# Kernel tuning notes

Measured on AMD Instinct MI355X. Metric: run time of the kernel, lower is better.

The kernel has to match this reference:

```python
import jax, jax.numpy as jnp
import numpy as np
from jax import lax

PAD_ID = 0
V, E = 100000, 300          # word vocab / embedding dim
VC, EC, C = 100, 50, 100    # char vocab / char emb dim / char conv channels
H, L = 256, 17              # lstm hidden / n_labels
B, S, LC = 32, 128, 50


def _conv1d(x, w, b):
    # x [B, Cin, T], w [Cout, Cin, K] -> valid conv
    y = lax.conv_general_dilated(x, w, window_strides=(1,), padding='VALID',
                                 dimension_numbers=('NCH', 'OIH', 'NCH'))
    return y + b[None, :, None]


def _lstm_dir(x_sbd, w_ih, w_hh, b, h0, c0):
    # x_sbd [S,B,D]; PyTorch gate order i,f,g,o
    def step(carry, x_t):
        h, c = carry
        g = x_t @ w_ih.T + h @ w_hh.T + b
        i, f, gg, o = jnp.split(g, 4, axis=-1)
        c = jax.nn.sigmoid(f) * c + jax.nn.sigmoid(i) * jnp.tanh(gg)
        h = jax.nn.sigmoid(o) * jnp.tanh(c)
        return (h, c), h
    _, hs = lax.scan(step, (h0, c0), x_sbd)
    return hs  # [S,B,H]


def _emissions(x, x_char, word_emb, char_emb,
               conv1_w, conv1_b, conv2_w, conv2_b, conv3_w, conv3_b,
               w_ih_f, w_hh_f, b_f, w_ih_b, w_hh_b, b_b, h0, c0, fc_w, fc_b):
    emb = word_emb[x]                                   # [B,S,E]
    ce = char_emb[x_char].transpose(0, 2, 1)            # [B,EC,LC]
    ce = jax.nn.relu(_conv1d(ce, conv1_w, conv1_b))
    ce = jax.nn.relu(_conv1d(ce, conv2_w, conv2_b))
    ce = jax.nn.relu(_conv1d(ce, conv3_w, conv3_b))
    pooled = ce.max(axis=2)                             # [B,C] (max over time)
    char_rep = jnp.broadcast_to(pooled[:, None, :], (emb.shape[0], emb.shape[1], pooled.shape[1]))
    xin = jnp.concatenate([emb, char_rep], axis=2)      # [B,S,E+C]
    xs = xin.transpose(1, 0, 2)                         # [S,B,D]
    hf = _lstm_dir(xs, w_ih_f, w_hh_f, b_f, h0[0], c0[0])
    hb = _lstm_dir(xs[::-1], w_ih_b, w_hh_b, b_b, h0[1], c0[1])[::-1]
    hcat = jnp.concatenate([hf, hb], axis=-1).transpose(1, 0, 2)  # [B,S,2H]
    em = hcat @ fc_w.T + fc_b                           # [B,S,L]
    return jax.nn.softmax(em, axis=1)                   # faithful: softmax over seq dim


def _viterbi(emissions, mask, start_t, trans, end_t):
    # emissions [B,S,L], mask [B,S]
    em = emissions.transpose(1, 0, 2)                   # [S,B,L]
    m = mask.T                                          # [S,B]
    score0 = start_t[None, :] + em[0]                   # [B,L]

    def fwd(score, inp):
        e_t, m_t = inp
        cand = score[:, :, None] + trans[None] + e_t[:, None, :]  # [B,L,L]
        nscore = cand.max(axis=1)
        idx = cand.argmax(axis=1).astype(jnp.int32)
        score = jnp.where(m_t[:, None] > 0, nscore, score)
        return score, idx

    score, hist = lax.scan(fwd, score0, (em[1:], m[1:]))  # hist [S-1,B,L]
    score = score + end_t[None, :]
    last = jnp.argmax(score, axis=-1).astype(jnp.int32)   # [B]

    def back(cur, inp):
        h_t, m_t = inp
        prev = jnp.take_along_axis(h_t, cur[:, None], axis=1)[:, 0]
        cur = jnp.where(m_t > 0, prev, cur)
        return cur, cur

    _, tags_rev = lax.scan(back, last, (hist[::-1], m[1:][::-1]))
    tags = jnp.concatenate([tags_rev[::-1], last[None]], axis=0)  # [S,B]
    return tags.T                                                 # [B,S]


def setup_inputs() -> dict:
    key = jax.random.key(0)
    ks = jax.random.split(key, 24)
    f = lambda i, shape, s=0.1: (jax.random.normal(ks[i], shape, dtype=jnp.float32) * s)
    inp = {
        'x': jax.random.randint(ks[0], (B, S), 1, V),          # no PAD -> mask all ones
        'x_char': jax.random.randint(ks[1], (B, LC), 1, VC),
        'word_emb': f(2, (V, E), 1.0),
        'char_emb': f(3, (VC, EC), 1.0).at[PAD_ID].set(0.0),
        'conv1_w': f(4, (C, EC, 3)), 'conv1_b': f(5, (C,)),
        'conv2_w': f(6, (C, C, 4)), 'conv2_b': f(7, (C,)),
        'conv3_w': f(8, (C, C, 5)), 'conv3_b': f(9, (C,)),
        'w_ih_f': f(10, (4 * H, E + C)), 'w_hh_f': f(11, (4 * H, H)), 'b_f': f(12, (4 * H,)),
        'w_ih_b': f(13, (4 * H, E + C)), 'w_hh_b': f(14, (4 * H, H)), 'b_b': f(15, (4 * H,)),
        'h0': f(16, (2, B, H), 1.0), 'c0': f(17, (2, B, H), 1.0),
        'fc_w': f(18, (L, 2 * H)), 'fc_b': f(19, (L,)),
        'start_t': f(20, (L,)), 'trans': f(21, (L, L)), 'end_t': f(22, (L,)),
    }
    return inp


def reference(x, x_char, word_emb, char_emb, conv1_w, conv1_b, conv2_w, conv2_b,
              conv3_w, conv3_b, w_ih_f, w_hh_f, b_f, w_ih_b, w_hh_b, b_b,
              h0, c0, fc_w, fc_b, start_t, trans, end_t):
    mask = (x != PAD_ID).astype(jnp.float32)
    em = _emissions(x, x_char, word_emb, char_emb, conv1_w, conv1_b, conv2_w, conv2_b,
                    conv3_w, conv3_b, w_ih_f, w_hh_f, b_f, w_ih_b, w_hh_b, b_b,
                    h0, c0, fc_w, fc_b)
    return _viterbi(em, mask, start_t, trans, end_t)
```

## Files before the change

kernel.cpp:

```cpp
#include <hip/hip_runtime.h>
#include <cmath>

#define B_   32
#define S_   128
#define E_   300
#define C_   100
#define EC_  50
#define LC_  50
#define H_   256
#define G4_  1024
#define L_   17
#define DHID_ 400
#define NBLKD 8
#define SLAB_ 8192
#define SENT2_ 0x7E007E00u

typedef _Float16 half8 __attribute__((ext_vector_type(8)));
typedef float f32x4 __attribute__((ext_vector_type(4)));
typedef unsigned long long ull;
struct __align__(16) U2 { ull x, y; };

__device__ __forceinline__ unsigned pack_split(float v) {
  _Float16 hi = (fabsf(v) >= 6.104e-5f) ? (_Float16)v : (_Float16)0.0f;
  float hif = (float)hi;
  _Float16 lo = (_Float16)((v - hif) * 2048.0f);
  return (unsigned)__builtin_bit_cast(unsigned short, hi)
       | ((unsigned)__builtin_bit_cast(unsigned short, lo) << 16);
}

__global__ void k_hinit(const float* __restrict__ h0, unsigned* __restrict__ hfrag) {
  int idx = blockIdx.x * 256 + threadIdx.x;
  const int total = 2 * (S_ + 1) * SLAB_;
  if (idx >= total) return;
  int sd = idx / SLAB_;
  int within = idx % SLAB_;
  int t = sd % (S_ + 1), d = sd / (S_ + 1);
  if (t != 0) { hfrag[idx] = SENT2_; return; }
  int m8 = within & 7;
  int lane = (within >> 3) & 63;
  int q = within >> 9;
  int Kt = q & 7, Nt = q >> 3;
  int m = m8 & 3, isLo = m8 >> 2;
  int k0 = Kt * 32 + (lane >> 4) * 8 + 2 * m;
  int b = Nt * 16 + (lane & 15);
  unsigned p0 = pack_split(h0[((size_t)d * B_ + b) * H_ + k0]);
  unsigned p1 = pack_split(h0[((size_t)d * B_ + b) * H_ + k0 + 1]);
  unsigned hiw = (p0 & 0xFFFFu) | (p1 << 16);
  unsigned low = (p0 >> 16) | (p1 & 0xFFFF0000u);
  hfrag[idx] = isLo ? low : hiw;
}

__global__ void k_conv1(const int* __restrict__ x_char, const float* __restrict__ char_emb,
                        const float* __restrict__ w1, const float* __restrict__ b1,
                        float* __restrict__ out1) {
  int b = blockIdx.x;
  int ot = blockIdx.y;
  __shared__ float ce[EC_ * 52];
  __shared__ float wl[50 * 150];
  __shared__ int ids[LC_];
  int tid = threadIdx.x;
  if (tid < LC_) ids[tid] = x_char[b * LC_ + tid];
  __syncthreads();
  for (int idx = tid; idx < LC_ * EC_; idx += 256) {
    int t = idx / EC_, ec = idx % EC_;
    ce[ec * 52 + t] = char_emb[ids[t] * EC_ + ec];
  }
  int obase = ot * 50;
  for (int idx = tid; idx < 50 * 150; idx += 256)
    wl[idx] = w1[obase * 150 + idx];
  __syncthreads();
  for (int idx = tid; idx < 50 * 48; idx += 256) {
    int o = idx / 48, t = idx % 48;
    float acc = b1[obase + o];
    const float* wr = &wl[o * 150];
    for (int c = 0; c < EC_; ++c) {
      const float* ip = &ce[c * 52 + t];
      acc += wr[c * 3 + 0] * ip[0] + wr[c * 3 + 1] * ip[1] + wr[c * 3 + 2] * ip[2];
    }
    out1[((size_t)b * C_ + obase + o) * 48 + t] = fmaxf(acc, 0.0f);
  }
}

__global__ void k_conv2(const float* __restrict__ in, const float* __restrict__ w2,
                        const float* __restrict__ b2, float* __restrict__ out2) {
  int b = blockIdx.x, ot = blockIdx.y;
  __shared__ float il[C_ * 48];
  __shared__ float wl[25 * 400];
  int tid = threadIdx.x;
  for (int idx = tid; idx < C_ * 48; idx += 256) il[idx] = in[(size_t)b * C_ * 48 + idx];
  int obase = ot * 25;
  for (int idx = tid; idx < 25 * 400; idx += 256) wl[idx] = w2[obase * 400 + idx];
  __syncthreads();
  for (int idx = tid; idx < 25 * 45; idx += 256) {
    int o = idx / 45, t = idx % 45;
    float acc = b2[obase + o];
    const float* wr = &wl[o * 400];
    for (int c = 0; c < C_; ++c) {
      const float* ip = &il[c * 48 + t];
      acc += wr[c * 4 + 0] * ip[0] + wr[c * 4 + 1] * ip[1] +
             wr[c * 4 + 2] * ip[2] + wr[c * 4 + 3] * ip[3];
    }
    out2[((size_t)b * C_ + obase + o) * 45 + t] = fmaxf(acc, 0.0f);
  }
}

__global__ void k_conv3(const float* __restrict__ in, const float* __restrict__ w3,
                        const float* __restrict__ b3, float* __restrict__ pooled) {
  int b = blockIdx.x, ot = blockIdx.y;
  __shared__ float il[C_ * 45];
  __shared__ float wl[20 * 500];
  __shared__ float o3[20 * 44];
  int tid = threadIdx.x;
  for (int idx = tid; idx < C_ * 45; idx += 256) il[idx] = in[(size_t)b * C_ * 45 + idx];
  int obase = ot * 20;
  for (int idx = tid; idx < 20 * 500; idx += 256) wl[idx] = w3[obase * 500 + idx];
  __syncthreads();
  for (int idx = tid; idx < 20 * 41; idx += 256) {
    int o = idx / 41, t = idx % 41;
    float acc = b3[obase + o];
    const float* wr = &wl[o * 500];
    for (int c = 0; c < C_; ++c) {
      const float* ip = &il[c * 45 + t];
      acc += wr[c * 5 + 0] * ip[0] + wr[c * 5 + 1] * ip[1] + wr[c * 5 + 2] * ip[2] +
             wr[c * 5 + 3] * ip[3] + wr[c * 5 + 4] * ip[4];
    }
    o3[o * 44 + t] = fmaxf(acc, 0.0f);
  }
  __syncthreads();
  if (tid < 20) {
    float m = o3[tid * 44];
    for (int t = 1; t < 41; ++t) m = fmaxf(m, o3[tid * 44 + t]);
    pooled[b * C_ + obase + tid] = m;
  }
}

__global__ void k_biaseff(const float* __restrict__ pooled,
                          const float* __restrict__ w_ih_f, const float* __restrict__ b_f,
                          const float* __restrict__ w_ih_b, const float* __restrict__ b_b,
                          float* __restrict__ biaseff) {
  int b = blockIdx.x, d = blockIdx.y;
  const float* wih = d ? w_ih_b : w_ih_f;
  const float* bb = d ? b_b : b_f;
  __shared__ float pl[C_];
  int tid = threadIdx.x;
  if (tid < C_) pl[tid] = pooled[b * C_ + tid];
  __syncthreads();
  for (int j = tid; j < G4_; j += 256) {
    float acc = bb[j];
    const float* wr = &wih[(size_t)j * DHID_ + E_];
    for (int c = 0; c < C_; ++c) acc += pl[c] * wr[c];
    biaseff[((size_t)d * G4_ + j) * B_ + b] = acc;
  }
}

__global__ __launch_bounds__(256) void k_gemm_in(
    const int* __restrict__ x, const float* __restrict__ word_emb,
    const float* __restrict__ w_ih_f, const float* __restrict__ w_ih_b,
    const float* __restrict__ biaseff, float* __restrict__ gi) {
  int jt = blockIdx.x;
  int rt = blockIdx.y;
  int d = blockIdx.z;
  const float* wih = d ? w_ih_b : w_ih_f;
  __shared__ float Al[16][132];
  __shared__ float Bl[16][132];
  __shared__ int wid[128];
  int tid = threadIdx.x;
  int r0 = rt * 128, j0 = jt * 128;
  if (tid < 128) {
    int r = r0 + tid;
    int t = r >> 5, b = r & 31;
    wid[tid] = x[b * S_ + t];
  }
  __syncthreads();
  float acc[8][8];
#pragma unroll
  for (int i = 0; i < 8; ++i)
#pragma unroll
    for (int j = 0; j < 8; ++j) acc[i][j] = 0.f;
  int ty = tid >> 4, tx = tid & 15;

  for (int k0 = 0; k0 < 304; k0 += 16) {
#pragma unroll
    for (int i = 0; i < 2; ++i) {
      int f = tid + i * 256;
      int rl = f >> 2, kc = f & 3;
      const float* src = word_emb + (size_t)wid[rl] * E_;
#pragma unroll
      for (int e = 0; e < 4; ++e) {
        int k = k0 + kc * 4 + e;
        float v = src[k < E_ ? k : (E_ - 1)];
        Al[kc * 4 + e][rl] = (k < E_) ? v : 0.f;
      }
    }
#pragma unroll
    for (int i = 0; i < 2; ++i) {
      int f = tid + i * 256;
      int jl = f >> 2, kc = f & 3;
      const float* src = wih + (size_t)(j0 + jl) * DHID_;
#pragma unroll
      for (int e = 0; e < 4; ++e) {
        int k = k0 + kc * 4 + e;
        float v = src[k];
        Bl[kc * 4 + e][jl] = (k < E_) ? v : 0.f;
      }
    }
    __syncthreads();
#pragma unroll
    for (int kk = 0; kk < 16; ++kk) {
      float4 a0 = *(const float4*)(&Al[kk][ty * 8]);
      float4 a1 = *(const float4*)(&Al[kk][ty * 8 + 4]);
      float4 b0 = *(const float4*)(&Bl[kk][tx * 8]);
      float4 b1 = *(const float4*)(&Bl[kk][tx * 8 + 4]);
      float av[8] = {a0.x, a0.y, a0.z, a0.w, a1.x, a1.y, a1.z, a1.w};
      float bv[8] = {b0.x, b0.y, b0.z, b0.w, b1.x, b1.y, b1.z, b1.w};
#pragma unroll
      for (int i = 0; i < 8; ++i)
#pragma unroll
        for (int j = 0; j < 8; ++j) acc[i][j] = fmaf(av[i], bv[j], acc[i][j]);
    }
    __syncthreads();
  }
  int b0 = (ty & 3) * 8;
  int tt = rt * 4 + (ty >> 2);
#pragma unroll
  for (int jj = 0; jj < 8; ++jj) {
    int j = j0 + tx * 8 + jj;
    const float* be = biaseff + ((size_t)d * G4_ + j) * B_ + b0;
    float4 bl = *(const float4*)(be);
    float4 bh = *(const float4*)(be + 4);
    float4 lo, hi;
    lo.x = acc[0][jj] + bl.x; lo.y = acc[1][jj] + bl.y;
    lo.z = acc[2][jj] + bl.z; lo.w = acc[3][jj] + bl.w;
    hi.x = acc[4][jj] + bh.x; hi.y = acc[5][jj] + bh.y;
    hi.z = acc[6][jj] + bh.z; hi.w = acc[7][jj] + bh.w;
    float* dst = gi + (((size_t)(d * S_ + tt) * G4_) + j) * B_ + b0;
    *(float4*)dst = lo;
    *(float4*)(dst + 4) = hi;
  }
}

__global__ __launch_bounds__(256, 1) void k_lstm(
    const float* __restrict__ w_hh_f, const float* __restrict__ w_hh_b,
    const float* __restrict__ c0, const float* __restrict__ gi,
    float* __restrict__ hbuf, unsigned* __restrict__ hfrag) {
  const int iblk = blockIdx.x;
  const int d = blockIdx.y;
  const float* whh = d ? w_hh_b : w_hh_f;
  const int tid = threadIdx.x;
  const int w = tid >> 6;
  const int l = tid & 63;
  const int lx = l & 15, lq = l >> 4;
  const int u0 = iblk * 32;

  __shared__ ull slh[2048];
  __shared__ ull sll[2048];
  __shared__ float gl[4 * 32 * 33];
  __shared__ unsigned ps[2 * 576];

  half8 whi[2][8], wlo[2][8];
#pragma unroll
  for (int Mt = 0; Mt < 2; ++Mt) {
#pragma unroll
    for (int Kt = 0; Kt < 8; ++Kt) {
      int row = w * H_ + u0 + Mt * 16 + lx;
      int kk0 = Kt * 32 + lq * 8;
      const float* src = whh + (size_t)row * H_ + kk0;
      float4 f0 = *(const float4*)src;
      float4 f1 = *(const float4*)(src + 4);
      float wv[8] = {f0.x, f0.y, f0.z, f0.w, f1.x, f1.y, f1.z, f1.w};
      union { unsigned short s[8]; half8 h; } HI, LO;
#pragma unroll
      for (int j = 0; j < 8; ++j) {
        float v = wv[j];
        _Float16 hi = (fabsf(v) >= 6.104e-5f) ? (_Float16)v : (_Float16)0.0f;
        float hif = (float)hi;
        _Float16 lo = (_Float16)((v - hif) * 2048.0f);
        HI.s[j] = __builtin_bit_cast(unsigned short, hi);
        LO.s[j] = __builtin_bit_cast(unsigned short, lo);
      }
      whi[Mt][Kt] = HI.h;
      wlo[Mt][Kt] = LO.h;
    }
  }

  const int bc = tid & 31, cw = tid >> 5;
  float creg[4];
#pragma unroll
  for (int cu = 0; cu < 4; ++cu)
    creg[cu] = c0[((size_t)d * B_ + bc) * H_ + u0 + cu * 8 + cw];

  const int pNt = bc >> 4;
  const int pm = cw >> 1;
  const bool phi = (cw & 1) == 0;
  const int plane = bc & 15;
  const float inv2048 = 1.0f / 2048.0f;

  for (int t = 0; t < S_; ++t) {
    int torig = d ? (S_ - 1 - t) : t;

    f32x4 acch[2][2], accl[2][2];
    {
      const float* gbase = gi + ((size_t)(d * S_ + torig) * G4_) * B_;
#pragma unroll
      for (int Mt = 0; Mt < 2; ++Mt)
#pragma unroll
        for (int Nt = 0; Nt < 2; ++Nt) {
          f32x4 v;
#pragma unroll
          for (int r = 0; r < 4; ++r) {
            int j = w * H_ + u0 + Mt * 16 + lq * 4 + r;
            v[r] = gbase[(size_t)j * B_ + Nt * 16 + lx];
          }
          acch[Mt][Nt] = v;
          f32x4 z = {0.f, 0.f, 0.f, 0.f};
          accl[Mt][Nt] = z;
        }
    }

    const ull* hp = (const ull*)(hfrag + (size_t)(d * (S_ + 1) + t) * SLAB_);
    ull pv[4][4];
#pragma unroll
    for (int c = 0; c < 4; ++c) {
      size_t base = ((size_t)(w * 4 + c) * 64 + l) * 4;
#pragma unroll
      for (int j = 0; j < 4; ++j)
        pv[c][j] = __hip_atomic_load(&hp[base + j], __ATOMIC_RELAXED,
                                     __HIP_MEMORY_SCOPE_AGENT);
    }
    for (;;) {
      bool pending = false;
#pragma unroll
      for (int c = 0; c < 4; ++c)
#pragma unroll
        for (int j = 0; j < 4; ++j)
          pending |= ((unsigned)pv[c][j] == SENT2_) |
                     ((unsigned)(pv[c][j] >> 32) == SENT2_);
      if (!pending) break;
#pragma unroll
      for (int c = 0; c < 4; ++c) {
        size_t base = ((size_t)(w * 4 + c) * 64 + l) * 4;
#pragma unroll
        for (int j = 0; j < 4; ++j)
          pv[c][j] = __hip_atomic_load(&hp[base + j], __ATOMIC_RELAXED,
                                       __HIP_MEMORY_SCOPE_AGENT);
      }
    }
#pragma unroll
    for (int c = 0; c < 4; ++c) {
      int idx = ((w * 4 + c) * 64 + l) * 2;
      U2 vh; vh.x = pv[c][0]; vh.y = pv[c][1];
      U2 vl; vl.x = pv[c][2]; vl.y = pv[c][3];
      *(U2*)&slh[idx] = vh;
      *(U2*)&sll[idx] = vl;
    }
    __syncthreads();

#pragma unroll
    for (int Kt = 0; Kt < 8; ++Kt) {
      half8 Bhi[2], Blo[2];
#pragma unroll
      for (int Nt = 0; Nt < 2; ++Nt) {
        int idx = ((Nt * 8 + Kt) * 64 + l) * 2;
        union { U2 u; half8 h; } UH, UL;
        UH.u = *(const U2*)&slh[idx];
        UL.u = *(const U2*)&sll[idx];
        Bhi[Nt] = UH.h;
        Blo[Nt] = UL.h;
      }
#pragma unroll
      for (int Mt = 0; Mt < 2; ++Mt)
#pragma unroll
        for (int Nt = 0; Nt < 2; ++Nt) {
          acch[Mt][Nt] = __builtin_amdgcn_mfma_f32_16x16x32_f16(
              whi[Mt][Kt], Bhi[Nt], acch[Mt][Nt], 0, 0, 0);
          accl[Mt][Nt] = __builtin_amdgcn_mfma_f32_16x16x32_f16(
              whi[Mt][Kt], Blo[Nt], accl[Mt][Nt], 0, 0, 0);
          accl[Mt][Nt] = __builtin_amdgcn_mfma_f32_16x16x32_f16(
              wlo[Mt][Kt], Bhi[Nt], accl[Mt][Nt], 0, 0, 0);
        }
    }

#pragma unroll
    for (int Mt = 0; Mt < 2; ++Mt)
#pragma unroll
      for (int Nt = 0; Nt < 2; ++Nt)
#pragma unroll
        for (int r = 0; r < 4; ++r) {
          int ul = Mt * 16 + lq * 4 + r;
          gl[(w * 32 + ul) * 33 + Nt * 16 + lx] =
              acch[Mt][Nt][r] + accl[Mt][Nt][r] * inv2048;
        }
    __syncthreads();

    float hreg[4];
#pragma unroll
    for (int cu = 0; cu < 4; ++cu) {
      int u = cu * 8 + cw;
      float g_i = gl[(0 * 32 + u) * 33 + bc];
      float g_f = gl[(1 * 32 + u) * 33 + bc];
      float g_g = gl[(2 * 32 + u) * 33 + bc];
      float g_o = gl[(3 * 32 + u) * 33 + bc];
      float si = 1.f / (1.f + __expf(-g_i));
      float sf = 1.f / (1.f + __expf(-g_f));
      float so = 1.f / (1.f + __expf(-g_o));
      float tg = 1.f - 2.f / (__expf(2.f * g_g) + 1.f);
      float cn = sf * creg[cu] + si * tg;
      float tc = 1.f - 2.f / (__expf(2.f * cn) + 1.f);
      float hn = so * tc;
      creg[cu] = cn;
      hreg[cu] = hn;
      unsigned me = pack_split(hn);
      unsigned pa = (unsigned)__shfl_xor((int)me, 32, 64);
      unsigned je = (cw & 1) ? pa : me;
      unsigned jo = (cw & 1) ? me : pa;
      unsigned hiw = (je & 0xFFFFu) | (jo << 16);
      unsigned low = (je >> 16) | (jo & 0xFFFF0000u);
      int lane2 = (cu << 4) | plane;
      int m8 = phi ? pm : (4 + pm);
      ps[pNt * 576 + lane2 * 9 + m8] = phi ? hiw : low;
    }
    __syncthreads();

    {
      ull* slab64 = (ull*)(hfrag + (size_t)(d * (S_ + 1) + t + 1) * SLAB_);
#pragma unroll
      for (int hh = 0; hh < 2; ++hh) {
        int r = tid;
        int Nt = hh;
        int lane2 = r >> 2, m2 = r & 3;
        unsigned a = ps[Nt * 576 + lane2 * 9 + 2 * m2];
        unsigned b = ps[Nt * 576 + lane2 * 9 + 2 * m2 + 1];
        ull v = (ull)a | ((ull)b << 32);
        __hip_atomic_store(&slab64[(size_t)(Nt * 8 + iblk) * 256 + r], v,
                           __ATOMIC_RELAXED, __HIP_MEMORY_SCOPE_AGENT);
      }
      float* hb = hbuf + (size_t)(d * (S_ + 1) + t + 1) * (H_ * B_) + u0 * B_;
#pragma unroll
      for (int cu = 0; cu < 4; ++cu) hb[cu * 256 + tid] = hreg[cu];
    }
  }
}

__global__ void k_fc(const float* __restrict__ hbuf, const float* __restrict__ fc_w,
                     const float* __restrict__ fc_b, float* __restrict__ em) {
  int idx = blockIdx.x * 256 + threadIdx.x;
  if (idx >= B_ * S_ * L_) return;
  int l = idx % L_;
  int bs = idx / L_;
  int s = bs % S_;
  int b = bs / S_;
  const float* hf = hbuf + ((size_t)(s + 1)) * (H_ * B_);
  const float* hb = hbuf + ((size_t)(S_ + 1) + (S_ - s)) * ((size_t)H_ * B_);
  const float* w = fc_w + (size_t)l * (2 * H_);
  float acc = fc_b[l];
  for (int k = 0; k < H_; ++k) acc = fmaf(hf[k * B_ + b], w[k], acc);
  for (int k = 0; k < H_; ++k) acc = fmaf(hb[k * B_ + b], w[H_ + k], acc);
  em[(size_t)idx] = acc;
}

__global__ void k_softmax(float* __restrict__ em) {
  int b = blockIdx.x;
  __shared__ float e[S_ * L_];
  int tid = threadIdx.x;
  for (int i = tid; i < S_ * L_; i += 256) e[i] = em[(size_t)b * S_ * L_ + i];
  __syncthreads();
  if (tid < L_) {
    int l = tid;
    float m = -INFINITY;
    for (int s = 0; s < S_; ++s) m = fmaxf(m, e[s * L_ + l]);
    float sum = 0.f;
    for (int s = 0; s < S_; ++s) {
      float ex = expf(e[s * L_ + l] - m);
      e[s * L_ + l] = ex;
      sum += ex;
    }
    for (int s = 0; s < S_; ++s) e[s * L_ + l] = e[s * L_ + l] / sum;
  }
  __syncthreads();
  for (int i = tid; i < S_ * L_; i += 256) em[(size_t)b * S_ * L_ + i] = e[i];
}

__global__ void k_viterbi(const float* __restrict__ em, const int* __restrict__ x,
                          const float* __restrict__ start_t, const float* __restrict__ trans,
                          const float* __restrict__ end_t, int* __restrict__ hist,
                          int* __restrict__ out) {
  int b = blockIdx.x;
  __shared__ float tr[L_ * L_];
  __shared__ float sc[2][L_];
  int tid = threadIdx.x;
  for (int i = tid; i < L_ * L_; i += 64) tr[i] = trans[i];
  if (tid < L_) sc[0][tid] = start_t[tid] + em[((size_t)b * S_ + 0) * L_ + tid];
  __syncthreads();
  int cbuf = 0;
  for (int t = 1; t < S_; ++t) {
    if (tid < L_) {
      int j = tid;
      float e = em[((size_t)b * S_ + t) * L_ + j];
      float best = -INFINITY;
      int arg = 0;
      for (int i = 0; i < L_; ++i) {
        float v = (sc[cbuf][i] + tr[i * L_ + j]) + e;
        if (v > best) { best = v; arg = i; }
      }
      int maskt = (x[b * S_ + t] != 0);
      sc[cbuf ^ 1][j] = maskt ? best : sc[cbuf][j];
      hist[((size_t)(t - 1) * B_ + b) * L_ + j] = arg;
    }
    __syncthreads();
    cbuf ^= 1;
  }
  __syncthreads();
  if (tid == 0) {
    float best = -INFINITY;
    int last = 0;
    for (int j = 0; j < L_; ++j) {
      float v = sc[cbuf][j] + end_t[j];
      if (v > best) { best = v; last = j; }
    }
    int cur = last;
    out[b * S_ + S_ - 1] = cur;
    for (int p = S_ - 2; p >= 0; --p) {
      if (x[b * S_ + p + 1] != 0) cur = hist[((size_t)p * B_ + b) * L_ + cur];
      out[b * S_ + p] = cur;
    }
  }
}

extern "C" void kernel_launch(void* const* d_in, const int* in_sizes, int n_in,
                              void* d_out, int out_size, void* d_ws, size_t ws_size,
                              hipStream_t stream) {
  const int* x        = (const int*)d_in[0];
  const int* x_char   = (const int*)d_in[1];
  const float* word_emb = (const float*)d_in[2];
  const float* char_emb = (const float*)d_in[3];
  const float* conv1_w = (const float*)d_in[4];
  const float* conv1_b = (const float*)d_in[5];
  const float* conv2_w = (const float*)d_in[6];
  const float* conv2_b = (const float*)d_in[7];
  const float* conv3_w = (const float*)d_in[8];
  const float* conv3_b = (const float*)d_in[9];
  const float* w_ih_f = (const float*)d_in[10];
  const float* w_hh_f = (const float*)d_in[11];
  const float* b_f    = (const float*)d_in[12];
  const float* w_ih_b = (const float*)d_in[13];
  const float* w_hh_b = (const float*)d_in[14];
  const float* b_b    = (const float*)d_in[15];
  const float* h0     = (const float*)d_in[16];
  const float* c0     = (const float*)d_in[17];
  const float* fc_w   = (const float*)d_in[18];
  const float* fc_b   = (const float*)d_in[19];
  const float* start_t = (const float*)d_in[20];
  const float* trans  = (const float*)d_in[21];
  const float* end_t  = (const float*)d_in[22];
  int* out = (int*)d_out;

  char* ws = (char*)d_ws;
  auto alloc = [&](size_t bytes) -> char* {
    char* p = ws;
    ws += (bytes + 1023) & ~(size_t)1023;
    return p;
  };
  float* pooled  = (float*)alloc(sizeof(float) * B_ * C_);
  float* biaseff = (float*)alloc(sizeof(float) * 2 * G4_ * B_);
  float* gi      = (float*)alloc(sizeof(float) * 2 * S_ * G4_ * B_);
  float* hbuf    = (float*)alloc(sizeof(float) * 2 * (S_ + 1) * H_ * B_);
  unsigned* hfrag = (unsigned*)alloc(sizeof(unsigned) * 2 * (S_ + 1) * SLAB_);
  float* out1    = (float*)alloc(sizeof(float) * B_ * C_ * 48);
  float* out2    = (float*)alloc(sizeof(float) * B_ * C_ * 45);
  float* em      = (float*)alloc(sizeof(float) * B_ * S_ * L_);
  int* hist      = (int*)alloc(sizeof(int) * (S_ - 1) * B_ * L_);

  const int hinit_total = 2 * (S_ + 1) * SLAB_;
  k_hinit<<<(hinit_total + 255) / 256, 256, 0, stream>>>(h0, hfrag);
  k_conv1<<<dim3(32, 2), 256, 0, stream>>>(x_char, char_emb, conv1_w, conv1_b, out1);
  k_conv2<<<dim3(32, 4), 256, 0, stream>>>(out1, conv2_w, conv2_b, out2);
  k_conv3<<<dim3(32, 5), 256, 0, stream>>>(out2, conv3_w, conv3_b, pooled);
  k_biaseff<<<dim3(32, 2), 256, 0, stream>>>(pooled, w_ih_f, b_f, w_ih_b, b_b, biaseff);
  k_gemm_in<<<dim3(8, 32, 2), 256, 0, stream>>>(x, word_emb, w_ih_f, w_ih_b, biaseff, gi);
  k_lstm<<<dim3(NBLKD, 2), 256, 0, stream>>>(w_hh_f, w_hh_b, c0, gi, hbuf, hfrag);
  k_fc<<<(B_ * S_ * L_ + 255) / 256, 256, 0, stream>>>(hbuf, fc_w, fc_b, em);
  k_softmax<<<32, 256, 0, stream>>>(em);
  k_viterbi<<<32, 64, 0, stream>>>(em, x, start_t, trans, end_t, hist, out);
}
```

Baseline: 1.052 ms.

## Use split-fp16 MFMA input GEMM, restructure FC, fuse softmax with Viterbi

Replaces the FP32 scalar input-projection GEMM with an MFMA 16x16x32 f16 GEMM. The GEMM uses hi/lo split-fp16 packing of weights and activations, and the pooled char features are folded into the K dimension, so the separate bias kernel is removed. The FC kernel is rewritten per timestep with transposed weights in shared memory and partial sums. Softmax and Viterbi are fused into one kernel that keeps emissions and backpointers in shared memory. This adds prep kernels and extra workspace traffic, and the split-fp16 trick may carry some precision risk.

```diff
diff --git a/kernel.cpp b/kernel.cpp
--- a/kernel.cpp
+++ b/kernel.cpp
@@ -14,6 +14,7 @@
 #define NBLKD 8
 #define SLAB_ 8192
 #define SENT2_ 0x7E007E00u
+#define KP_   208
 
 typedef _Float16 half8 __attribute__((ext_vector_type(8)));
 typedef float f32x4 __attribute__((ext_vector_type(4)));
@@ -134,108 +135,123 @@
   }
 }
 
-__global__ void k_biaseff(const float* __restrict__ pooled,
-                          const float* __restrict__ w_ih_f, const float* __restrict__ b_f,
-                          const float* __restrict__ w_ih_b, const float* __restrict__ b_b,
-                          float* __restrict__ biaseff) {
-  int b = blockIdx.x, d = blockIdx.y;
-  const float* wih = d ? w_ih_b : w_ih_f;
-  const float* bb = d ? b_b : b_f;
-  __shared__ float pl[C_];
-  int tid = threadIdx.x;
-  if (tid < C_) pl[tid] = pooled[b * C_ + tid];
-  __syncthreads();
-  for (int j = tid; j < G4_; j += 256) {
-    float acc = bb[j];
-    const float* wr = &wih[(size_t)j * DHID_ + E_];
-    for (int c = 0; c < C_; ++c) acc += pl[c] * wr[c];
-    biaseff[((size_t)d * G4_ + j) * B_ + b] = acc;
-  }
-}
-
-__global__ __launch_bounds__(256) void k_gemm_in(
-    const int* __restrict__ x, const float* __restrict__ word_emb,
-    const float* __restrict__ w_ih_f, const float* __restrict__ w_ih_b,
-    const float* __restrict__ biaseff, float* __restrict__ gi) {
-  int jt = blockIdx.x;
-  int rt = blockIdx.y;
-  int d = blockIdx.z;
-  const float* wih = d ? w_ih_b : w_ih_f;
-  __shared__ float Al[16][132];
-  __shared__ float Bl[16][132];
-  __shared__ int wid[128];
-  int tid = threadIdx.x;
-  int r0 = rt * 128, j0 = jt * 128;
-  if (tid < 128) {
-    int r = r0 + tid;
-    int t = r >> 5, b = r & 31;
-    wid[tid] = x[b * S_ + t];
-  }
-  __syncthreads();
-  float acc[8][8];
-#pragma unroll
-  for (int i = 0; i < 8; ++i)
-#pragma unroll
-    for (int j = 0; j < 8; ++j) acc[i][j] = 0.f;
-  int ty = tid >> 4, tx = tid & 15;
-
-  for (int k0 = 0; k0 < 304; k0 += 16) {
-#pragma unroll
-    for (int i = 0; i < 2; ++i) {
-      int f = tid + i * 256;
-      int rl = f >> 2, kc = f & 3;
-      const float* src = word_emb + (size_t)wid[rl] * E_;
-#pragma unroll
-      for (int e = 0; e < 4; ++e) {
-        int k = k0 + kc * 4 + e;
-        float v = src[k < E_ ? k : (E_ - 1)];
-        Al[kc * 4 + e][rl] = (k < E_) ? v : 0.f;
+__global__ void k_prep_w(const float* __restrict__ wf, const float* __restrict__ wb,
+                         unsigned* __restrict__ apH, unsigned* __restrict__ apL) {
+  int idx = blockIdx.x * 256 + threadIdx.x;
+  if (idx >= 2 * G4_ * KP_) return;
+  int d = idx / (G4_ * KP_);
+  int rem = idx % (G4_ * KP_);
+  int j = rem / KP_, k2 = rem % KP_;
+  const float* w = d ? wb : wf;
+  float v0 = 0.f, v1 = 0.f;
+  if (k2 < 200) { v0 = w[(size_t)j * DHID_ + 2 * k2]; v1 = w[(size_t)j * DHID_ + 2 * k2 + 1]; }
+  unsigned p0 = pack_split(v0), p1 = pack_split(v1);
+  apH[idx] = (p0 & 0xFFFFu) | (p1 << 16);
+  apL[idx] = (p0 >> 16) | (p1 & 0xFFFF0000u);
+}
+
+__global__ void k_prep_b(const int* __restrict__ x, const float* __restrict__ word_emb,
+                         const float* __restrict__ pooled,
+                         unsigned* __restrict__ bpH, unsigned* __restrict__ bpL) {
+  int r = blockIdx.x;
+  int k2 = threadIdx.x;
+  if (k2 >= KP_) return;
+  int t = r >> 5, b = r & 31;
+  float v0 = 0.f, v1 = 0.f;
+  if (k2 < 150) {
+    const float* e = word_emb + (size_t)x[b * S_ + t] * E_;
+    v0 = e[2 * k2]; v1 = e[2 * k2 + 1];
+  } else if (k2 < 200) {
+    v0 = pooled[b * C_ + 2 * k2 - 300];
+    v1 = pooled[b * C_ + 2 * k2 - 299];
+  }
+  unsigned p0 = pack_split(v0), p1 = pack_split(v1);
+  bpH[(size_t)r * KP_ + k2] = (p0 & 0xFFFFu) | (p1 << 16);
+  bpL[(size_t)r * KP_ + k2] = (p0 >> 16) | (p1 & 0xFFFF0000u);
+}
+
+__global__ __launch_bounds__(256) void k_gemm(
+    const unsigned* __restrict__ apH, const unsigned* __restrict__ apL,
+    const unsigned* __restrict__ bpH, const unsigned* __restrict__ bpL,
+    const float* __restrict__ b_f, const float* __restrict__ b_b,
+    float* __restrict__ gi) {
+  const int jt = blockIdx.x, rt = blockIdx.y, d = blockIdx.z;
+  const int j0 = jt * 128, r0 = rt * 128;
+  const int tid = threadIdx.x;
+  const int w = tid >> 6, l = tid & 63;
+  const int lx = l & 15, lq = l >> 4;
+
+  __shared__ unsigned aH[2048], aL[2048], bH[2048], bL[2048];
+
+  f32x4 acch[2][8], accl[2][8];
+#pragma unroll
+  for (int mt = 0; mt < 2; ++mt)
+#pragma unroll
+    for (int nt = 0; nt < 8; ++nt) {
+      f32x4 z = {0.f, 0.f, 0.f, 0.f};
+      acch[mt][nt] = z; accl[mt][nt] = z;
+    }
+
+  const int jr = tid >> 1, hh = tid & 1;
+  const int q_st = jr >> 4, lane_lo = jr & 15;
+  const unsigned* arH = apH + ((size_t)(d * G4_ + j0 + jr)) * KP_ + hh * 8;
+  const unsigned* arL = apL + ((size_t)(d * G4_ + j0 + jr)) * KP_ + hh * 8;
+  const unsigned* brH = bpH + ((size_t)(r0 + jr)) * KP_ + hh * 8;
+  const unsigned* brL = bpL + ((size_t)(r0 + jr)) * KP_ + hh * 8;
+  const int w0 = (q_st * 64 + lane_lo + 32 * hh) * 4;
+  const int w1 = (q_st * 64 + lane_lo + 32 * hh + 16) * 4;
+
+  for (int Kt = 0; Kt < 13; ++Kt) {
+    uint4 a0 = *(const uint4*)(arH + Kt * 16);
+    uint4 a1 = *(const uint4*)(arH + Kt * 16 + 4);
+    uint4 c0 = *(const uint4*)(arL + Kt * 16);
+    uint4 c1 = *(const uint4*)(arL + Kt * 16 + 4);
+    uint4 e0 = *(const uint4*)(brH + Kt * 16);
+    uint4 e1 = *(const uint4*)(brH + Kt * 16 + 4);
+    uint4 f0 = *(const uint4*)(brL + Kt * 16);
+    uint4 f1 = *(const uint4*)(brL + Kt * 16 + 4);
+    *(uint4*)&aH[w0] = a0; *(uint4*)&aH[w1] = a1;
+    *(uint4*)&aL[w0] = c0; *(uint4*)&aL[w1] = c1;
+    *(uint4*)&bH[w0] = e0; *(uint4*)&bH[w1] = e1;
+    *(uint4*)&bL[w0] = f0; *(uint4*)&bL[w1] = f1;
+    __syncthreads();
+
+    union u4h { uint4 u; half8 h; };
+    u4h AH0, AH1, AL0, AL1;
+    AH0.u = *(const uint4*)&aH[((2 * w + 0) * 64 + l) * 4];
+    AH1.u = *(const uint4*)&aH[((2 * w + 1) * 64 + l) * 4];
+    AL0.u = *(const uint4*)&aL[((2 * w + 0) * 64 + l) * 4];
+    AL1.u = *(const uint4*)&aL[((2 * w + 1) * 64 + l) * 4];
+#pragma unroll
+    for (int nt = 0; nt < 8; ++nt) {
+      u4h BHn, BLn;
+      BHn.u = *(const uint4*)&bH[(nt * 64 + l) * 4];
+      BLn.u = *(const uint4*)&bL[(nt * 64 + l) * 4];
+      acch[0][nt] = __builtin_amdgcn_mfma_f32_16x16x32_f16(AH0.h, BHn.h, acch[0][nt], 0, 0, 0);
+      accl[0][nt] = __builtin_amdgcn_mfma_f32_16x16x32_f16(AH0.h, BLn.h, accl[0][nt], 0, 0, 0);
+      accl[0][nt] = __builtin_amdgcn_mfma_f32_16x16x32_f16(AL0.h, BHn.h, accl[0][nt], 0, 0, 0);
+      acch[1][nt] = __builtin_amdgcn_mfma_f32_16x16x32_f16(AH1.h, BHn.h, acch[1][nt], 0, 0, 0);
+      accl[1][nt] = __builtin_amdgcn_mfma_f32_16x16x32_f16(AH1.h, BLn.h, accl[1][nt], 0, 0, 0);
+      accl[1][nt] = __builtin_amdgcn_mfma_f32_16x16x32_f16(AL1.h, BHn.h, accl[1][nt], 0, 0, 0);
+    }
+    __syncthreads();
+  }
+
+  const float* bias = d ? b_b : b_f;
+  const float inv2048 = 1.0f / 2048.0f;
+#pragma unroll
+  for (int mt = 0; mt < 2; ++mt) {
+#pragma unroll
+    for (int nt = 0; nt < 8; ++nt) {
+      int rr = r0 + nt * 16 + lx;
+      int tt = rr >> 5, bb = rr & 31;
+      float* dst = gi + ((size_t)(d * S_ + tt) * G4_) * B_ + bb;
+#pragma unroll
+      for (int r4 = 0; r4 < 4; ++r4) {
+        int j = j0 + (2 * w + mt) * 16 + lq * 4 + r4;
+        dst[(size_t)j * B_] = acch[mt][nt][r4] + accl[mt][nt][r4] * inv2048 + bias[j];
       }
     }
-#pragma unroll
-    for (int i = 0; i < 2; ++i) {
-      int f = tid + i * 256;
-      int jl = f >> 2, kc = f & 3;
-      const float* src = wih + (size_t)(j0 + jl) * DHID_;
-#pragma unroll
-      for (int e = 0; e < 4; ++e) {
-        int k = k0 + kc * 4 + e;
-        float v = src[k];
-        Bl[kc * 4 + e][jl] = (k < E_) ? v : 0.f;
-      }
-    }
-    __syncthreads();
-#pragma unroll
-    for (int kk = 0; kk < 16; ++kk) {
-      float4 a0 = *(const float4*)(&Al[kk][ty * 8]);
-      float4 a1 = *(const float4*)(&Al[kk][ty * 8 + 4]);
-      float4 b0 = *(const float4*)(&Bl[kk][tx * 8]);
-      float4 b1 = *(const float4*)(&Bl[kk][tx * 8 + 4]);
-      float av[8] = {a0.x, a0.y, a0.z, a0.w, a1.x, a1.y, a1.z, a1.w};
-      float bv[8] = {b0.x, b0.y, b0.z, b0.w, b1.x, b1.y, b1.z, b1.w};
-#pragma unroll
-      for (int i = 0; i < 8; ++i)
-#pragma unroll
-        for (int j = 0; j < 8; ++j) acc[i][j] = fmaf(av[i], bv[j], acc[i][j]);
-    }
-    __syncthreads();
-  }
-  int b0 = (ty & 3) * 8;
-  int tt = rt * 4 + (ty >> 2);
-#pragma unroll
-  for (int jj = 0; jj < 8; ++jj) {
-    int j = j0 + tx * 8 + jj;
-    const float* be = biaseff + ((size_t)d * G4_ + j) * B_ + b0;
-    float4 bl = *(const float4*)(be);
-    float4 bh = *(const float4*)(be + 4);
-    float4 lo, hi;
-    lo.x = acc[0][jj] + bl.x; lo.y = acc[1][jj] + bl.y;
-    lo.z = acc[2][jj] + bl.z; lo.w = acc[3][jj] + bl.w;
-    hi.x = acc[4][jj] + bh.x; hi.y = acc[5][jj] + bh.y;
-    hi.z = acc[6][jj] + bh.z; hi.w = acc[7][jj] + bh.w;
-    float* dst = gi + (((size_t)(d * S_ + tt) * G4_) + j) * B_ + b0;
-    *(float4*)dst = lo;
-    *(float4*)(dst + 4) = hi;
   }
 }
 
@@ -424,9 +440,9 @@
     {
       ull* slab64 = (ull*)(hfrag + (size_t)(d * (S_ + 1) + t + 1) * SLAB_);
 #pragma unroll
-      for (int hh = 0; hh < 2; ++hh) {
+      for (int hh2 = 0; hh2 < 2; ++hh2) {
         int r = tid;
-        int Nt = hh;
+        int Nt = hh2;
         int lane2 = r >> 2, m2 = r & 3;
         unsigned a = ps[Nt * 576 + lane2 * 9 + 2 * m2];
         unsigned b = ps[Nt * 576 + lane2 * 9 + 2 * m2 + 1];
@@ -441,28 +457,55 @@
   }
 }
 
-__global__ void k_fc(const float* __restrict__ hbuf, const float* __restrict__ fc_w,
-                     const float* __restrict__ fc_b, float* __restrict__ em) {
-  int idx = blockIdx.x * 256 + threadIdx.x;
-  if (idx >= B_ * S_ * L_) return;
-  int l = idx % L_;
-  int bs = idx / L_;
-  int s = bs % S_;
-  int b = bs / S_;
-  const float* hf = hbuf + ((size_t)(s + 1)) * (H_ * B_);
-  const float* hb = hbuf + ((size_t)(S_ + 1) + (S_ - s)) * ((size_t)H_ * B_);
-  const float* w = fc_w + (size_t)l * (2 * H_);
-  float acc = fc_b[l];
-  for (int k = 0; k < H_; ++k) acc = fmaf(hf[k * B_ + b], w[k], acc);
-  for (int k = 0; k < H_; ++k) acc = fmaf(hb[k * B_ + b], w[H_ + k], acc);
-  em[(size_t)idx] = acc;
-}
-
-__global__ void k_softmax(float* __restrict__ em) {
+__global__ __launch_bounds__(256) void k_fc(const float* __restrict__ hbuf,
+                                            const float* __restrict__ fc_w,
+                                            const float* __restrict__ fc_b,
+                                            float* __restrict__ em) {
+  const int s = blockIdx.x;
+  const int tid = threadIdx.x;
+  __shared__ float wT[512 * 18];
+  __shared__ float psum[256 * 18];
+  for (int i = tid; i < L_ * 512; i += 256) {
+    int l = i / 512, k = i % 512;
+    wT[k * 18 + l] = fc_w[i];
+  }
+  __syncthreads();
+  const int b = tid & 31, kq = tid >> 5;
+  const float* hf = hbuf + (size_t)(s + 1) * (H_ * B_);
+  const float* hbk = hbuf + (size_t)(S_ + 1 + (S_ - s)) * (H_ * B_);
+  float acc[L_];
+#pragma unroll
+  for (int l = 0; l < L_; ++l) acc[l] = 0.f;
+  for (int i = 0; i < 64; ++i) {
+    int k = kq * 64 + i;
+    float hv = (k < 256) ? hf[k * 32 + b] : hbk[(k - 256) * 32 + b];
+    const float* wr = &wT[k * 18];
+#pragma unroll
+    for (int l = 0; l < L_; ++l) acc[l] = fmaf(hv, wr[l], acc[l]);
+  }
+#pragma unroll
+  for (int l = 0; l < L_; ++l) psum[tid * 18 + l] = acc[l];
+  __syncthreads();
+  for (int idx = tid; idx < B_ * L_; idx += 256) {
+    int bb = idx & 31, l = idx >> 5;
+    float sum = fc_b[l];
+    for (int q = 0; q < 8; ++q) sum += psum[(q * 32 + bb) * 18 + l];
+    em[((size_t)bb * S_ + s) * L_ + l] = sum;
+  }
+}
+
+__global__ void k_smv(const float* __restrict__ em, const int* __restrict__ x,
+                      const float* __restrict__ start_t, const float* __restrict__ trans,
+                      const float* __restrict__ end_t, int* __restrict__ out) {
   int b = blockIdx.x;
+  int tid = threadIdx.x;
   __shared__ float e[S_ * L_];
-  int tid = threadIdx.x;
-  for (int i = tid; i < S_ * L_; i += 256) e[i] = em[(size_t)b * S_ * L_ + i];
+  __shared__ float tr[L_ * L_];
+  __shared__ float sc[2][L_];
+  __shared__ int hist[(S_ - 1) * L_];
+  __shared__ int tags[S_];
+  for (int i = tid; i < S_ * L_; i += 64) e[i] = em[(size_t)b * S_ * L_ + i];
+  for (int i = tid; i < L_ * L_; i += 64) tr[i] = trans[i];
   __syncthreads();
   if (tid < L_) {
     int l = tid;
@@ -477,39 +520,26 @@
     for (int s = 0; s < S_; ++s) e[s * L_ + l] = e[s * L_ + l] / sum;
   }
   __syncthreads();
-  for (int i = tid; i < S_ * L_; i += 256) em[(size_t)b * S_ * L_ + i] = e[i];
-}
-
-__global__ void k_viterbi(const float* __restrict__ em, const int* __restrict__ x,
-                          const float* __restrict__ start_t, const float* __restrict__ trans,
-                          const float* __restrict__ end_t, int* __restrict__ hist,
-                          int* __restrict__ out) {
-  int b = blockIdx.x;
-  __shared__ float tr[L_ * L_];
-  __shared__ float sc[2][L_];
-  int tid = threadIdx.x;
-  for (int i = tid; i < L_ * L_; i += 64) tr[i] = trans[i];
-  if (tid < L_) sc[0][tid] = start_t[tid] + em[((size_t)b * S_ + 0) * L_ + tid];
+  if (tid < L_) sc[0][tid] = start_t[tid] + e[tid];
   __syncthreads();
   int cbuf = 0;
   for (int t = 1; t < S_; ++t) {
     if (tid < L_) {
       int j = tid;
-      float e = em[((size_t)b * S_ + t) * L_ + j];
+      float ev = e[t * L_ + j];
       float best = -INFINITY;
       int arg = 0;
       for (int i = 0; i < L_; ++i) {
-        float v = (sc[cbuf][i] + tr[i * L_ + j]) + e;
+        float v = (sc[cbuf][i] + tr[i * L_ + j]) + ev;
         if (v > best) { best = v; arg = i; }
       }
       int maskt = (x[b * S_ + t] != 0);
       sc[cbuf ^ 1][j] = maskt ? best : sc[cbuf][j];
-      hist[((size_t)(t - 1) * B_ + b) * L_ + j] = arg;
+      hist[(t - 1) * L_ + j] = arg;
     }
     __syncthreads();
     cbuf ^= 1;
   }
-  __syncthreads();
   if (tid == 0) {
     float best = -INFINITY;
     int last = 0;
@@ -518,12 +548,14 @@
       if (v > best) { best = v; last = j; }
     }
     int cur = last;
-    out[b * S_ + S_ - 1] = cur;
+    tags[S_ - 1] = cur;
     for (int p = S_ - 2; p >= 0; --p) {
-      if (x[b * S_ + p + 1] != 0) cur = hist[((size_t)p * B_ + b) * L_ + cur];
-      out[b * S_ + p] = cur;
-    }
-  }
+      if (x[b * S_ + p + 1] != 0) cur = hist[p * L_ + cur];
+      tags[p] = cur;
+    }
+  }
+  __syncthreads();
+  for (int s = tid; s < S_; s += 64) out[b * S_ + s] = tags[s];
 }
 
 extern "C" void kernel_launch(void* const* d_in, const int* in_sizes, int n_in,
@@ -561,24 +593,26 @@
     return p;
   };
   float* pooled  = (float*)alloc(sizeof(float) * B_ * C_);
-  float* biaseff = (float*)alloc(sizeof(float) * 2 * G4_ * B_);
   float* gi      = (float*)alloc(sizeof(float) * 2 * S_ * G4_ * B_);
   float* hbuf    = (float*)alloc(sizeof(float) * 2 * (S_ + 1) * H_ * B_);
   unsigned* hfrag = (unsigned*)alloc(sizeof(unsigned) * 2 * (S_ + 1) * SLAB_);
+  unsigned* apH  = (unsigned*)alloc(sizeof(unsigned) * 2 * G4_ * KP_);
+  unsigned* apL  = (unsigned*)alloc(sizeof(unsigned) * 2 * G4_ * KP_);
+  unsigned* bpH  = (unsigned*)alloc(sizeof(unsigned) * 4096 * KP_);
+  unsigned* bpL  = (unsigned*)alloc(sizeof(unsigned) * 4096 * KP_);
   float* out1    = (float*)alloc(sizeof(float) * B_ * C_ * 48);
   float* out2    = (float*)alloc(sizeof(float) * B_ * C_ * 45);
   float* em      = (float*)alloc(sizeof(float) * B_ * S_ * L_);
-  int* hist      = (int*)alloc(sizeof(int) * (S_ - 1) * B_ * L_);
 
   const int hinit_total = 2 * (S_ + 1) * SLAB_;
   k_hinit<<<(hinit_total + 255) / 256, 256, 0, stream>>>(h0, hfrag);
+  k_prep_w<<<(2 * G4_ * KP_ + 255) / 256, 256, 0, stream>>>(w_ih_f, w_ih_b, apH, apL);
   k_conv1<<<dim3(32, 2), 256, 0, stream>>>(x_char, char_emb, conv1_w, conv1_b, out1);
   k_conv2<<<dim3(32, 4), 256, 0, stream>>>(out1, conv2_w, conv2_b, out2);
   k_conv3<<<dim3(32, 5), 256, 0, stream>>>(out2, conv3_w, conv3_b, pooled);
-  k_biaseff<<<dim3(32, 2), 256, 0, stream>>>(pooled, w_ih_f, b_f, w_ih_b, b_b, biaseff);
-  k_gemm_in<<<dim3(8, 32, 2), 256, 0, stream>>>(x, word_emb, w_ih_f, w_ih_b, biaseff, gi);
+  k_prep_b<<<4096, 256, 0, stream>>>(x, word_emb, pooled, bpH, bpL);
+  k_gemm<<<dim3(8, 32, 2), 256, 0, stream>>>(apH, apL, bpH, bpL, b_f, b_b, gi);
   k_lstm<<<dim3(NBLKD, 2), 256, 0, stream>>>(w_hh_f, w_hh_b, c0, gi, hbuf, hfrag);
-  k_fc<<<(B_ * S_ * L_ + 255) / 256, 256, 0, stream>>>(hbuf, fc_w, fc_b, em);
-  k_softmax<<<32, 256, 0, stream>>>(em);
-  k_viterbi<<<32, 64, 0, stream>>>(em, x, start_t, trans, end_t, hist, out);
-}
+  k_fc<<<S_, 256, 0, stream>>>(hbuf, fc_w, fc_b, em);
+  k_smv<<<B_, 64, 0, stream>>>(em, x, start_t, trans, end_t, out);
+}
```

New measurement: 928.4 us. 1.13x faster.
